# Kernel optimization log

Measured on AMD Instinct MI355X. Metric: run time of the kernel, lower is better.

The kernel has to match this reference:

```python
import jax, jax.numpy as jnp
import numpy as np
import math

D_MODEL = 1024
NUM_HEADS = 16
D_KEY = D_MODEL // NUM_HEADS  # 64, used only for the softmax scale
B, S = 4, 2048


def setup_inputs() -> dict:
    key = jax.random.key(0)
    ks = jax.random.split(key, 7)
    scale = 1.0 / math.sqrt(D_MODEL)
    x = jax.random.normal(ks[0], (B, S, D_MODEL), dtype=jnp.float32)
    # torch.nn.Linear params: weight [out, in], bias [out]
    Wq = jax.random.normal(ks[1], (D_MODEL, D_MODEL), dtype=jnp.float32) * scale
    bq = jax.random.normal(ks[2], (D_MODEL,), dtype=jnp.float32) * scale
    Wk = jax.random.normal(ks[3], (D_MODEL, D_MODEL), dtype=jnp.float32) * scale
    bk = jax.random.normal(ks[4], (D_MODEL,), dtype=jnp.float32) * scale
    Wv = jax.random.normal(ks[5], (D_MODEL, D_MODEL), dtype=jnp.float32) * scale
    bv = jax.random.normal(ks[6], (D_MODEL,), dtype=jnp.float32) * scale
    return {"x": x, "Wq": Wq, "bq": bq, "Wk": Wk, "bk": bk, "Wv": Wv, "bv": bv}


def reference(x, Wq, bq, Wk, bk, Wv, bv):
    # Q, K, V projections (torch Linear: x @ W.T + b)
    Q = jnp.einsum('bsd,ed->bse', x, Wq) + bq  # [B,S,D]
    K = jnp.einsum('bsd,ed->bse', x, Wk) + bk
    V = jnp.einsum('bsd,ed->bse', x, Wv) + bv
    inv_sqrt_dk = 1.0 / math.sqrt(D_KEY)
    # full-width attention (no head split, as in the source forward)
    scores = jnp.einsum('bqd,bkd->bqk', Q, K) * inv_sqrt_dk  # [B,S,S]
    weights = jax.nn.softmax(scores, axis=-1)
    return jnp.einsum('bqk,bkd->bqd', weights, V)  # [B,S,D]
```

## Files before the change

### kernel.cpp

```cpp
#include <hip/hip_runtime.h>
#include <stdint.h>

#define S_LEN 2048
#define DMODEL 1024
#define NBATCH 4
#define MROWS (NBATCH * S_LEN)

typedef __bf16 bf16x8 __attribute__((ext_vector_type(8)));
typedef float f32x4 __attribute__((ext_vector_type(4)));

__device__ __forceinline__ unsigned short f2bf(float f) {
  unsigned int x = __builtin_bit_cast(unsigned int, f);
  x += 0x7FFFu + ((x >> 16) & 1u);
  return (unsigned short)(x >> 16);
}

template <int N>
__device__ __forceinline__ void waitvm() {
  static_assert(N <= 8, "vmcnt range");
  if constexpr (N < 0) {}
  else if constexpr (N == 0) asm volatile("s_waitcnt vmcnt(0)" ::: "memory");
  else if constexpr (N == 1) asm volatile("s_waitcnt vmcnt(1)" ::: "memory");
  else if constexpr (N == 2) asm volatile("s_waitcnt vmcnt(2)" ::: "memory");
  else if constexpr (N == 3) asm volatile("s_waitcnt vmcnt(3)" ::: "memory");
  else if constexpr (N == 4) asm volatile("s_waitcnt vmcnt(4)" ::: "memory");
  else if constexpr (N == 5) asm volatile("s_waitcnt vmcnt(5)" ::: "memory");
  else if constexpr (N == 6) asm volatile("s_waitcnt vmcnt(6)" ::: "memory");
  else if constexpr (N == 7) asm volatile("s_waitcnt vmcnt(7)" ::: "memory");
  else asm volatile("s_waitcnt vmcnt(8)" ::: "memory");
}
#define BARRIER() do { __builtin_amdgcn_s_barrier(); asm volatile("" ::: "memory"); } while (0)
#define LGKM0() do { asm volatile("s_waitcnt lgkmcnt(0)" ::: "memory"); \
                     __builtin_amdgcn_sched_barrier(0); } while (0)

__global__ void cvt_kernel(const float* __restrict__ src, ushort4* __restrict__ dst, int n4) {
  int i = blockIdx.x * blockDim.x + threadIdx.x;
  if (i < n4) {
    float4 v = reinterpret_cast<const float4*>(src)[i];
    ushort4 o;
    o.x = f2bf(v.x); o.y = f2bf(v.y); o.z = f2bf(v.z); o.w = f2bf(v.w);
    dst[i] = o;
  }
}

__global__ void prep_kernel(const float* __restrict__ Wq, const float* __restrict__ Wk,
                            const float* __restrict__ Wv, const float* __restrict__ bq,
                            const float* __restrict__ bk, ushort4* __restrict__ Wqkb,
                            ushort4* __restrict__ Wvb, float4* __restrict__ bqk) {
  const int NW = DMODEL * DMODEL / 4;
  int i = blockIdx.x * blockDim.x + threadIdx.x;
  float4 v;
  if (i < NW) v = reinterpret_cast<const float4*>(Wq)[i];
  else if (i < 2 * NW) v = reinterpret_cast<const float4*>(Wk)[i - NW];
  else v = reinterpret_cast<const float4*>(Wv)[i - 2 * NW];
  ushort4 o;
  o.x = f2bf(v.x); o.y = f2bf(v.y); o.z = f2bf(v.z); o.w = f2bf(v.w);
  if (i < 2 * NW) Wqkb[i] = o;
  else Wvb[i - 2 * NW] = o;
  if (i < 512) bqk[i] = (i < 256) ? reinterpret_cast<const float4*>(bq)[i]
                                  : reinterpret_cast<const float4*>(bk)[i - 256];
}

template <int BM_, int EP, int NT>
__global__ __launch_bounds__(512, 2) void gemm8(
    const unsigned short* __restrict__ A, const unsigned short* __restrict__ Bm,
    void* __restrict__ Cp, const float* __restrict__ bias,
    int lda, int ldb, int ldc, float scale,
    long zsA, long zsB, long zsC) {
  constexpr int BN_ = 256;
  constexpr int BK = 64;
  constexpr int RA = BM_ / 128;
  constexpr int HALF_A = (BM_ / 2) * 128;
  constexpr int HALF_B = 128 * 128;
  constexpr int ATILE = BM_ * 128;
  constexpr int BTILE = BN_ * 128;
  constexpr int MREP = BM_ / 32;
  constexpr int MQ = MREP / 2;
  constexpr int VPRO = (BM_ == 256) ? 4 : 3;
  constexpr int V_P0 = (BM_ == 256) ? 4 : 2;
  constexpr int V_P3 = (BM_ == 256) ? 8 : 6;
  constexpr int V_P5 = (BM_ == 256) ? 4 : 3;
  constexpr int VD_P0 = (BM_ == 256) ? 2 : 1;

  __shared__ alignas(16) char lds[(ATILE + BTILE) * 2];

  const int tid = threadIdx.x;
  const int l = tid & 63;
  const int w = tid >> 6;
  const int wm = w >> 2;
  const int wn = w & 3;

  const int gx = gridDim.x;
  const int nwg = gridDim.x * gridDim.y;
  int n = blockIdx.y * gx + blockIdx.x;
  int n2 = (n & 7) * (nwg >> 3) + (n >> 3);
  const int tileM = (n2 / gx) * BM_;
  const int tileN = (n2 % gx) * BN_;

  const int z = blockIdx.z;
  const unsigned short* Ab = A + (size_t)z * zsA;
  const unsigned short* Bb = Bm + (size_t)z * zsB;

  const int srow = l >> 3;
  const int scol = (((l & 7) ^ srow) * 16);

  auto stageA = [&](int buf, int t, int h) {
#pragma unroll
    for (int r = 0; r < RA; ++r) {
      int row = h * (BM_ / 2) + r * 64 + w * 8 + srow;
      const char* g = (const char*)(Ab + (size_t)(tileM + row) * lda + t * BK) + scol;
      char* d = lds + buf * (ATILE + BTILE) + h * HALF_A + r * 8192 + w * 1024;
      __builtin_amdgcn_global_load_lds(
          (const __attribute__((address_space(1))) void*)g,
          (__attribute__((address_space(3))) void*)d, 16, 0, 0);
    }
  };
  auto stageB = [&](int buf, int t, int h) {
#pragma unroll
    for (int r = 0; r < 2; ++r) {
      int row = h * 128 + r * 64 + w * 8 + srow;
      const char* g = (const char*)(Bb + (size_t)(tileN + row) * ldb + t * BK) + scol;
      char* d = lds + buf * (ATILE + BTILE) + ATILE + h * HALF_B + r * 8192 + w * 1024;
      __builtin_amdgcn_global_load_lds(
          (const __attribute__((address_space(1))) void*)g,
          (__attribute__((address_space(3))) void*)d, 16, 0, 0);
    }
  };

  f32x4 acc[MREP][4];
#pragma unroll
  for (int m = 0; m < MREP; ++m)
#pragma unroll
    for (int nn = 0; nn < 4; ++nn) acc[m][nn] = f32x4{0.f, 0.f, 0.f, 0.f};

  const int frow = l & 15;
  auto rdA = [&](int buf, int mh, int m, int kk) -> bf16x8 {
    int row = mh * (BM_ / 2) + wm * (BM_ / 4) + m * 16 + frow;
    int col = (kk * 64 + ((l >> 4) * 16)) ^ ((row & 7) << 4);
    return *reinterpret_cast<const bf16x8*>(lds + buf * (ATILE + BTILE) + row * 128 + col);
  };
  auto rdB = [&](int buf, int nh, int nn, int kk) -> bf16x8 {
    int row = nh * 128 + wn * 32 + nn * 16 + frow;
    int col = (kk * 64 + ((l >> 4) * 16)) ^ ((row & 7) << 4);
    return *reinterpret_cast<const bf16x8*>(lds + buf * (ATILE + BTILE) + ATILE + row * 128 + col);
  };

  bf16x8 avA[MQ], avB[MQ];
  bf16x8 bvv[2][2][2];

  auto rdAset = [&](int buf, int mh, int kk, bf16x8 (&dst)[MQ]) {
#pragma unroll
    for (int m = 0; m < MQ; ++m) dst[m] = rdA(buf, mh, m, kk);
  };
  auto rdBset = [&](int buf, int nh, int kk) {
#pragma unroll
    for (int nn = 0; nn < 2; ++nn) bvv[nh][kk][nn] = rdB(buf, nh, nn, kk);
  };
  auto mf8 = [&](bf16x8 (&av)[MQ], int mh, int nh, int kk) {
    __builtin_amdgcn_s_setprio(1);
#pragma unroll
    for (int m = 0; m < MQ; ++m)
#pragma unroll
      for (int nn = 0; nn < 2; ++nn)
        acc[mh * MQ + m][nh * 2 + nn] = __builtin_amdgcn_mfma_f32_16x16x32_bf16(
            av[m], bvv[nh][kk][nn], acc[mh * MQ + m][nh * 2 + nn], 0, 0, 0);
    __builtin_amdgcn_s_setprio(0);
  };

  stageA(0, 0, 0);
  stageB(0, 0, 0);
  stageB(0, 0, 1);
  stageA(0, 0, 1);
  waitvm<VPRO>();
  BARRIER();

#pragma unroll 2
  for (int t = 0; t < NT - 1; ++t) {
    const int buf = t & 1, nb = buf ^ 1;
    rdAset(buf, 0, 0, avA); rdBset(buf, 0, 0);
    stageA(nb, t + 1, 0); waitvm<V_P0>(); BARRIER(); LGKM0();
    mf8(avA, 0, 0, 0);
    rdBset(buf, 1, 0);
    stageB(nb, t + 1, 0); BARRIER(); LGKM0();
    mf8(avA, 0, 1, 0);
    rdAset(buf, 0, 1, avB); rdBset(buf, 1, 1);
    stageB(nb, t + 1, 1); BARRIER(); LGKM0();
    mf8(avB, 0, 1, 1);
    rdBset(buf, 0, 1);
    stageA(nb, t + 1, 1); waitvm<V_P3>(); BARRIER(); LGKM0();
    mf8(avB, 0, 0, 1);
    rdAset(buf, 1, 1, avA);
    BARRIER(); LGKM0();
    mf8(avA, 1, 0, 1); mf8(avA, 1, 1, 1);
    rdAset(buf, 1, 0, avB);
    waitvm<V_P5>(); BARRIER(); LGKM0();
    mf8(avB, 1, 1, 0); mf8(avB, 1, 0, 0);
  }
  {
    const int buf = (NT - 1) & 1;
    rdAset(buf, 0, 0, avA); rdBset(buf, 0, 0); waitvm<VD_P0>(); BARRIER(); LGKM0();
    mf8(avA, 0, 0, 0);
    rdBset(buf, 1, 0); BARRIER(); LGKM0();
    mf8(avA, 0, 1, 0);
    rdAset(buf, 0, 1, avB); rdBset(buf, 1, 1); BARRIER(); LGKM0();
    mf8(avB, 0, 1, 1);
    rdBset(buf, 0, 1); waitvm<0>(); BARRIER(); LGKM0();
    mf8(avB, 0, 0, 1);
    rdAset(buf, 1, 1, avA); BARRIER(); LGKM0();
    mf8(avA, 1, 0, 1); mf8(avA, 1, 1, 1);
    rdAset(buf, 1, 0, avB); BARRIER(); LGKM0();
    mf8(avB, 1, 1, 0); mf8(avB, 1, 0, 0);
  }

  const int lr = (l >> 4) * 4;
  const int lc = l & 15;
#pragma unroll
  for (int mh = 0; mh < 2; ++mh) {
#pragma unroll
    for (int m = 0; m < MQ; ++m) {
#pragma unroll
      for (int nh = 0; nh < 2; ++nh) {
#pragma unroll
        for (int nn = 0; nn < 2; ++nn) {
          int gr = tileM + mh * (BM_ / 2) + wm * (BM_ / 4) + m * 16 + lr;
          int gc = tileN + nh * 128 + wn * 32 + nn * 16 + lc;
          f32x4 v = acc[mh * MQ + m][nh * 2 + nn];
          if constexpr (EP == 0 || EP == 3) {
            unsigned short* C = (unsigned short*)Cp + (size_t)z * zsC;
#pragma unroll
            for (int j = 0; j < 4; ++j) {
              float bb = (EP == 0) ? bias[gc] : bias[gr + j];
              C[(size_t)(gr + j) * ldc + gc] = f2bf(v[j] + bb);
            }
          } else {
            float* C = (float*)Cp + (size_t)z * zsC;
#pragma unroll
            for (int j = 0; j < 4; ++j)
              C[(size_t)(gr + j) * ldc + gc] = (EP == 1) ? v[j] * scale : v[j];
          }
        }
      }
    }
  }
}

__global__ __launch_bounds__(256) void softmax_kernel(const float* __restrict__ Sb,
                                                      unsigned short* __restrict__ P) {
  const size_t row = blockIdx.x;
  const float* sp = Sb + row * S_LEN;
  const int t = threadIdx.x;
  const int wid = t >> 6, lane = t & 63;
  float4 v0 = reinterpret_cast<const float4*>(sp)[t * 2];
  float4 v1 = reinterpret_cast<const float4*>(sp)[t * 2 + 1];
  float s[8] = {v0.x, v0.y, v0.z, v0.w, v1.x, v1.y, v1.z, v1.w};
  float mx = s[0];
#pragma unroll
  for (int i = 1; i < 8; ++i) mx = fmaxf(mx, s[i]);
#pragma unroll
  for (int o = 32; o > 0; o >>= 1) mx = fmaxf(mx, __shfl_xor(mx, o));
  __shared__ float redm[4];
  __shared__ float reds[4];
  if (lane == 0) redm[wid] = mx;
  __syncthreads();
  mx = fmaxf(fmaxf(redm[0], redm[1]), fmaxf(redm[2], redm[3]));
  float e[8];
  float sum = 0.f;
#pragma unroll
  for (int i = 0; i < 8; ++i) { e[i] = __expf(s[i] - mx); sum += e[i]; }
#pragma unroll
  for (int o = 32; o > 0; o >>= 1) sum += __shfl_xor(sum, o);
  if (lane == 0) reds[wid] = sum;
  __syncthreads();
  sum = reds[0] + reds[1] + reds[2] + reds[3];
  float inv = 1.0f / sum;
  ushort4 o0, o1;
  o0.x = f2bf(e[0] * inv); o0.y = f2bf(e[1] * inv); o0.z = f2bf(e[2] * inv); o0.w = f2bf(e[3] * inv);
  o1.x = f2bf(e[4] * inv); o1.y = f2bf(e[5] * inv); o1.z = f2bf(e[6] * inv); o1.w = f2bf(e[7] * inv);
  ushort4* dp = reinterpret_cast<ushort4*>(P + row * S_LEN);
  dp[t * 2] = o0;
  dp[t * 2 + 1] = o1;
}

extern "C" void kernel_launch(void* const* d_in, const int* in_sizes, int n_in,
                              void* d_out, int out_size, void* d_ws, size_t ws_size,
                              hipStream_t stream) {
  (void)in_sizes; (void)n_in; (void)out_size;
  const float* x = (const float*)d_in[0];
  const float* Wq = (const float*)d_in[1];
  const float* bq = (const float*)d_in[2];
  const float* Wk = (const float*)d_in[3];
  const float* bk = (const float*)d_in[4];
  const float* Wv = (const float*)d_in[5];
  const float* bv = (const float*)d_in[6];
  float* out = (float*)d_out;

  if (ws_size < 141557760ull) return;
  char* ws = (char*)d_ws;
  unsigned short* xb   = (unsigned short*)(ws);
  unsigned short* Wqkb = (unsigned short*)(ws + 16777216);
  unsigned short* Wvb  = (unsigned short*)(ws + 20971520);
  float*          bqk  = (float*)(ws + 23068672);
  unsigned short* QKb  = (unsigned short*)(ws + 24117248);
  float*          Sb   = (float*)(ws + 57671680);
  unsigned short* Vt   = (unsigned short*)(ws + 124780544);
  unsigned short* P    = QKb;

  cvt_kernel<<<dim3(MROWS * DMODEL / 4 / 256), 256, 0, stream>>>(x, (ushort4*)xb, MROWS * DMODEL / 4);
  prep_kernel<<<dim3(3 * DMODEL * DMODEL / 4 / 256), 256, 0, stream>>>(
      Wq, Wk, Wv, bq, bk, (ushort4*)Wqkb, (ushort4*)Wvb, (float4*)bqk);

  gemm8<256, 0, 16><<<dim3(8, 32, 1), 512, 0, stream>>>(
      xb, Wqkb, QKb, bqk, 1024, 1024, 2048, 1.f, 0, 0, 0);

  gemm8<128, 3, 16><<<dim3(8, 8, 4), 512, 0, stream>>>(
      Wvb, xb, Vt, bv, 1024, 1024, 2048, 1.f,
      0, (long)S_LEN * DMODEL, (long)DMODEL * S_LEN);

  gemm8<256, 1, 16><<<dim3(8, 8, 4), 512, 0, stream>>>(
      QKb, QKb + 1024, Sb, nullptr, 2048, 2048, 2048, 0.125f,
      (long)S_LEN * 2048, (long)S_LEN * 2048, (long)S_LEN * S_LEN);

  softmax_kernel<<<dim3(MROWS), 256, 0, stream>>>(Sb, P);

  gemm8<128, 2, 32><<<dim3(4, 16, 4), 512, 0, stream>>>(
      P, Vt, out, nullptr, 2048, 2048, 1024, 1.f,
      (long)S_LEN * S_LEN, (long)DMODEL * S_LEN, (long)S_LEN * DMODEL);
}
```

Before: 167.7 us.

## Restructure GEMM main loop into three phases with full-K fragment reads

Reorganizes the software-pipelined GEMM inner loop from six barrier-separated phases into three. Each phase now loads A and B fragments for both k-halves at once and issues twice as many MFMAs between barriers. New vmcnt wait thresholds are set to match the regrouped global-to-LDS staging. This removes barriers and LDS wait points per K-step, at the cost of more live fragment registers and coarser interleaving of loads with compute. In the final epilogue iteration, the last A read for the second half is preceded by an LDS wait but no barrier.

```diff
diff --git a/kernel.cpp b/kernel.cpp
--- a/kernel.cpp
+++ b/kernel.cpp
@@ -77,10 +77,10 @@
   constexpr int MREP = BM_ / 32;
   constexpr int MQ = MREP / 2;
   constexpr int VPRO = (BM_ == 256) ? 4 : 3;
-  constexpr int V_P0 = (BM_ == 256) ? 4 : 2;
-  constexpr int V_P3 = (BM_ == 256) ? 8 : 6;
-  constexpr int V_P5 = (BM_ == 256) ? 4 : 3;
-  constexpr int VD_P0 = (BM_ == 256) ? 2 : 1;
+  constexpr int W_PA = (BM_ == 256) ? 6 : 4;
+  constexpr int W_PB = (BM_ == 256) ? 6 : 5;
+  constexpr int W_PC = (BM_ == 256) ? 4 : 3;
+  constexpr int VDA  = (BM_ == 256) ? 2 : 1;
 
   __shared__ alignas(16) char lds[(ATILE + BTILE) * 2];
 
@@ -145,25 +145,31 @@
     return *reinterpret_cast<const bf16x8*>(lds + buf * (ATILE + BTILE) + ATILE + row * 128 + col);
   };
 
-  bf16x8 avA[MQ], avB[MQ];
-  bf16x8 bvv[2][2][2];
-
-  auto rdAset = [&](int buf, int mh, int kk, bf16x8 (&dst)[MQ]) {
-#pragma unroll
-    for (int m = 0; m < MQ; ++m) dst[m] = rdA(buf, mh, m, kk);
-  };
-  auto rdBset = [&](int buf, int nh, int kk) {
-#pragma unroll
-    for (int nn = 0; nn < 2; ++nn) bvv[nh][kk][nn] = rdB(buf, nh, nn, kk);
-  };
-  auto mf8 = [&](bf16x8 (&av)[MQ], int mh, int nh, int kk) {
+  bf16x8 avF[MQ][2];
+  bf16x8 bv0[2][2], bv1[2][2];
+
+  auto rdAfull = [&](int buf, int mh) {
+#pragma unroll
+    for (int m = 0; m < MQ; ++m)
+#pragma unroll
+      for (int kk = 0; kk < 2; ++kk) avF[m][kk] = rdA(buf, mh, m, kk);
+  };
+  auto rdBfull = [&](int buf, int nh, bf16x8 (&bv)[2][2]) {
+#pragma unroll
+    for (int nn = 0; nn < 2; ++nn)
+#pragma unroll
+      for (int kk = 0; kk < 2; ++kk) bv[nn][kk] = rdB(buf, nh, nn, kk);
+  };
+  auto mfc = [&](int mh, bf16x8 (&bv)[2][2], int nh) {
     __builtin_amdgcn_s_setprio(1);
 #pragma unroll
     for (int m = 0; m < MQ; ++m)
 #pragma unroll
       for (int nn = 0; nn < 2; ++nn)
-        acc[mh * MQ + m][nh * 2 + nn] = __builtin_amdgcn_mfma_f32_16x16x32_bf16(
-            av[m], bvv[nh][kk][nn], acc[mh * MQ + m][nh * 2 + nn], 0, 0, 0);
+#pragma unroll
+        for (int kk = 0; kk < 2; ++kk)
+          acc[mh * MQ + m][nh * 2 + nn] = __builtin_amdgcn_mfma_f32_16x16x32_bf16(
+              avF[m][kk], bv[nn][kk], acc[mh * MQ + m][nh * 2 + nn], 0, 0, 0);
     __builtin_amdgcn_s_setprio(0);
   };
 
@@ -177,39 +183,30 @@
 #pragma unroll 2
   for (int t = 0; t < NT - 1; ++t) {
     const int buf = t & 1, nb = buf ^ 1;
-    rdAset(buf, 0, 0, avA); rdBset(buf, 0, 0);
-    stageA(nb, t + 1, 0); waitvm<V_P0>(); BARRIER(); LGKM0();
-    mf8(avA, 0, 0, 0);
-    rdBset(buf, 1, 0);
-    stageB(nb, t + 1, 0); BARRIER(); LGKM0();
-    mf8(avA, 0, 1, 0);
-    rdAset(buf, 0, 1, avB); rdBset(buf, 1, 1);
-    stageB(nb, t + 1, 1); BARRIER(); LGKM0();
-    mf8(avB, 0, 1, 1);
-    rdBset(buf, 0, 1);
-    stageA(nb, t + 1, 1); waitvm<V_P3>(); BARRIER(); LGKM0();
-    mf8(avB, 0, 0, 1);
-    rdAset(buf, 1, 1, avA);
-    BARRIER(); LGKM0();
-    mf8(avA, 1, 0, 1); mf8(avA, 1, 1, 1);
-    rdAset(buf, 1, 0, avB);
-    waitvm<V_P5>(); BARRIER(); LGKM0();
-    mf8(avB, 1, 1, 0); mf8(avB, 1, 0, 0);
+    rdAfull(buf, 0); rdBfull(buf, 0, bv0);
+    stageA(nb, t + 1, 0); stageB(nb, t + 1, 0);
+    waitvm<W_PA>(); BARRIER(); LGKM0();
+    mfc(0, bv0, 0);
+    rdBfull(buf, 1, bv1);
+    stageB(nb, t + 1, 1);
+    waitvm<W_PB>(); BARRIER(); LGKM0();
+    mfc(0, bv1, 1);
+    rdAfull(buf, 1);
+    stageA(nb, t + 1, 1);
+    waitvm<W_PC>(); BARRIER(); LGKM0();
+    mfc(1, bv1, 1); mfc(1, bv0, 0);
   }
   {
     const int buf = (NT - 1) & 1;
-    rdAset(buf, 0, 0, avA); rdBset(buf, 0, 0); waitvm<VD_P0>(); BARRIER(); LGKM0();
-    mf8(avA, 0, 0, 0);
-    rdBset(buf, 1, 0); BARRIER(); LGKM0();
-    mf8(avA, 0, 1, 0);
-    rdAset(buf, 0, 1, avB); rdBset(buf, 1, 1); BARRIER(); LGKM0();
-    mf8(avB, 0, 1, 1);
-    rdBset(buf, 0, 1); waitvm<0>(); BARRIER(); LGKM0();
-    mf8(avB, 0, 0, 1);
-    rdAset(buf, 1, 1, avA); BARRIER(); LGKM0();
-    mf8(avA, 1, 0, 1); mf8(avA, 1, 1, 1);
-    rdAset(buf, 1, 0, avB); BARRIER(); LGKM0();
-    mf8(avB, 1, 1, 0); mf8(avB, 1, 0, 0);
+    rdAfull(buf, 0); rdBfull(buf, 0, bv0);
+    waitvm<VDA>(); BARRIER(); LGKM0();
+    mfc(0, bv0, 0);
+    rdBfull(buf, 1, bv1);
+    waitvm<0>(); BARRIER(); LGKM0();
+    mfc(0, bv1, 1);
+    rdAfull(buf, 1);
+    LGKM0();
+    mfc(1, bv1, 1); mfc(1, bv0, 0);
   }
 
   const int lr = (l >> 4) * 4;
```

Measured after the change: 165.9 us. About the same (-1.0%).
